# Kernel optimization log

Measured on AMD Instinct MI355X. Metric: run time of the kernel, lower is better.

The kernel has to match this reference:

```python
import jax, jax.numpy as jnp
import numpy as np

EPS = 1e-8  # matches Keras K.l2_normalize epsilon behavior closely enough for fp32

def _l2_normalize(x, axis=-1):
    # Keras l2_normalize: x / sqrt(max(sum(x^2), epsilon))
    sq = jnp.sum(jnp.square(x), axis=axis, keepdims=True)
    return x * jax.lax.rsqrt(jnp.maximum(sq, EPS))

def setup_inputs() -> dict:
    key = jax.random.key(0)
    k1, k2 = jax.random.split(key)
    matrix_1 = jax.random.normal(k1, (8, 2048, 128), dtype=jnp.float32)
    matrix_2 = jax.random.normal(k2, (8, 2048, 128), dtype=jnp.float32)
    return {"matrix_1": matrix_1, "matrix_2": matrix_2}

def reference(matrix_1, matrix_2):
    # Cosine similarity between every row pair: normalize then batched matmul.
    # Mathematically identical to tiling both matrices to (B, R1, R2, D) and
    # computing an elementwise cosine similarity, but without materializing tiles.
    m1 = _l2_normalize(matrix_1, axis=-1)  # (B, R1, D)
    m2 = _l2_normalize(matrix_2, axis=-1)  # (B, R2, D)
    return jnp.einsum('bid,bjd->bij', m1, m2)  # (B, R1, R2)
```

## Files before the change

kernel.cpp:

```cpp
#include <hip/hip_runtime.h>
#include <hip/hip_bf16.h>

#define BATCH 8
#define RROWS 2048
#define DDIM  128
#define BM    128
#define BN    64

using f32x4 = __attribute__((ext_vector_type(4))) float;
using s16x8 = __attribute__((ext_vector_type(8))) short;
using u16x4 = __attribute__((ext_vector_type(4))) unsigned short;

#define SCHED0() __builtin_amdgcn_sched_barrier(0)
#define LGKM0()  asm volatile("s_waitcnt lgkmcnt(0)" ::: "memory")

__device__ __forceinline__ unsigned short f2bf(float f) {
    unsigned int u = __builtin_bit_cast(unsigned int, f);
    u += 0x7fffu + ((u >> 16) & 1u);
    return (unsigned short)(u >> 16);
}

__device__ __forceinline__ u16x4 norm_cvt(float4 v) {
    float s = v.x * v.x + v.y * v.y + v.z * v.z + v.w * v.w;
    #pragma unroll
    for (int i = 1; i <= 16; i <<= 1) s += __shfl_xor(s, i);
    const float r = rsqrtf(fmaxf(s, 1e-8f));
    u16x4 p;
    p[0] = f2bf(v.x * r); p[1] = f2bf(v.y * r);
    p[2] = f2bf(v.z * r); p[3] = f2bf(v.w * r);
    return p;
}

__global__ __launch_bounds__(256, 2) void fused_kernel(const float* __restrict__ m1,
                                                       const float* __restrict__ m2,
                                                       float* __restrict__ out) {
    __shared__ __align__(16) char lds[32768];
    char* Bs0 = lds;
    char* Bs1 = lds + 16384;

    const int tid    = threadIdx.x;
    const int wave   = tid >> 6;
    const int lane   = tid & 63;
    const int l32    = tid & 31;
    const int grp    = tid >> 5;
    const int lid    = blockIdx.x;
    const int b      = lid & 7;
    const int idx    = lid >> 3;
    const int tile_m = idx >> 2;
    const int q      = idx & 3;

    const float* gA = m1 + ((size_t)b * RROWS + (size_t)tile_m * BM) * DDIM;
    const float* gB = m2 + ((size_t)b * RROWS + (size_t)q * 512) * DDIM;

    float4 rb[8];
    #pragma unroll
    for (int i = 0; i < 8; ++i)
        rb[i] = *(const float4*)(gB + (size_t)(i * 8 + grp) * DDIM + l32 * 4);

    #pragma unroll
    for (int s = 0; s < 16; ++s) {
        const int r = s * 8 + grp;
        const float4 va = *(const float4*)(gA + (size_t)r * DDIM + l32 * 4);
        const u16x4 pa = norm_cvt(va);
        const int off = r * 256 + l32 * 8;
        *(u16x4*)(lds + (off ^ ((r & 7) << 4))) = pa;
    }
    LGKM0();
    __builtin_amdgcn_s_barrier();

    const int wr   = wave >> 1;
    const int wc   = wave & 1;
    const int lrow = lane & 15;
    const int kb   = (lane >> 4) * 8;

    s16x8 af[4][4];
    #pragma unroll
    for (int kk = 0; kk < 4; ++kk) {
        const int k = kk * 32 + kb;
        #pragma unroll
        for (int m = 0; m < 4; ++m) {
            const int ra   = wr * 64 + m * 16 + lrow;
            const int offa = ra * 256 + k * 2;
            af[kk][m] = *(const s16x8*)(lds + (offa ^ ((ra & 7) << 4)));
        }
    }
    LGKM0();
    __builtin_amdgcn_s_barrier();

    #pragma unroll
    for (int i = 0; i < 8; ++i) {
        const int r = i * 8 + grp;
        const u16x4 pb = norm_cvt(rb[i]);
        const int off = r * 256 + l32 * 8;
        *(u16x4*)(Bs0 + (off ^ ((r & 7) << 4))) = pb;
    }
    #pragma unroll
    for (int i = 0; i < 8; ++i)
        rb[i] = *(const float4*)(gB + (size_t)(64 + i * 8 + grp) * DDIM + l32 * 4);
    LGKM0();
    __builtin_amdgcn_s_barrier();

    float* gout_base = out + (size_t)b * RROWS * RROWS
                           + (size_t)(tile_m * BM) * RROWS + (size_t)q * 512;

    #pragma unroll
    for (int t = 0; t < 8; ++t) {
        const char* Bs  = (t & 1) ? Bs1 : Bs0;
        char*       Bsn = (t & 1) ? Bs0 : Bs1;

        f32x4 acc[4][2];
        #pragma unroll
        for (int m = 0; m < 4; ++m)
            #pragma unroll
            for (int n = 0; n < 2; ++n)
                acc[m][n] = f32x4{0.f, 0.f, 0.f, 0.f};

        #pragma unroll
        for (int kk = 0; kk < 4; ++kk) {
            const int k = kk * 32 + kb;
            s16x8 bfr[2];
            #pragma unroll
            for (int n = 0; n < 2; ++n) {
                const int rbr  = wc * 32 + n * 16 + lrow;
                const int offb = rbr * 256 + k * 2;
                bfr[n] = *(const s16x8*)(Bs + (offb ^ ((rbr & 7) << 4)));
            }
            #pragma unroll
            for (int m = 0; m < 4; ++m)
                #pragma unroll
                for (int n = 0; n < 2; ++n)
                    acc[m][n] = __builtin_amdgcn_mfma_f32_16x16x32_bf16(af[kk][m], bfr[n], acc[m][n], 0, 0, 0);
        }

        float* gout = gout_base + t * BN;
        const int orow0 = wr * 64 + (lane >> 4) * 4;
        const int ocol0 = wc * 32 + lrow;
        #pragma unroll
        for (int m = 0; m < 4; ++m) {
            #pragma unroll
            for (int n = 0; n < 2; ++n) {
                const int col = ocol0 + n * 16;
                #pragma unroll
                for (int reg = 0; reg < 4; ++reg) {
                    const int row = orow0 + m * 16 + reg;
                    gout[(size_t)row * RROWS + col] = acc[m][n][reg];
                }
            }
        }

        if (t < 7) {
            SCHED0();
            #pragma unroll
            for (int i = 0; i < 8; ++i) {
                const int r = i * 8 + grp;
                const u16x4 pb = norm_cvt(rb[i]);
                const int off = r * 256 + l32 * 8;
                *(u16x4*)(Bsn + (off ^ ((r & 7) << 4))) = pb;
            }
            if (t < 6) {
                #pragma unroll
                for (int i = 0; i < 8; ++i)
                    rb[i] = *(const float4*)(gB + (size_t)((t + 2) * 64 + i * 8 + grp) * DDIM + l32 * 4);
            }
            LGKM0();
            __builtin_amdgcn_s_barrier();
        }
    }
}

extern "C" void kernel_launch(void* const* d_in, const int* in_sizes, int n_in,
                              void* d_out, int out_size, void* d_ws, size_t ws_size,
                              hipStream_t stream) {
    (void)in_sizes; (void)n_in; (void)out_size; (void)d_ws; (void)ws_size;
    const float* m1 = (const float*)d_in[0];
    const float* m2 = (const float*)d_in[1];
    float* out = (float*)d_out;

    fused_kernel<<<dim3(BATCH * (RROWS / BM) * (RROWS / BN / 8)), dim3(256), 0, stream>>>(m1, m2, out);
}
```

Baseline: 32.72 us.

## Double-buffer B register prefetch and normalize next tile before output stores

Splits the B-tile staging registers into two alternating buffers. Each iteration issues the global load for tile t+2 before the MFMA work, then normalizes and writes tile t+1 into LDS before the output stores, with scheduling barriers keeping that order. The goal is more latency hiding for B loads and less time where LDS writes wait behind global stores. In exchange the kernel holds 32 more VGPRs per thread, which could cause spills or hurt occupancy under the launch bounds of 2 blocks.

```diff
diff --git a/kernel.cpp b/kernel.cpp
--- a/kernel.cpp
+++ b/kernel.cpp
@@ -31,6 +31,20 @@
     return p;
 }
 
+#define LOAD_RB(RB, TI)                                                              \
+    _Pragma("unroll")                                                                \
+    for (int i = 0; i < 8; ++i)                                                      \
+        RB[i] = *(const float4*)(gB + (size_t)((TI) * 64 + i * 8 + grp) * DDIM + l32 * 4);
+
+#define PROCESS_RB(RB, DST)                                                          \
+    _Pragma("unroll")                                                                \
+    for (int i = 0; i < 8; ++i) {                                                    \
+        const int r_ = i * 8 + grp;                                                  \
+        const u16x4 pb_ = norm_cvt(RB[i]);                                           \
+        const int off_ = r_ * 256 + l32 * 8;                                         \
+        *(u16x4*)((DST) + (off_ ^ ((r_ & 7) << 4))) = pb_;                           \
+    }
+
 __global__ __launch_bounds__(256, 2) void fused_kernel(const float* __restrict__ m1,
                                                        const float* __restrict__ m2,
                                                        float* __restrict__ out) {
@@ -52,10 +66,8 @@
     const float* gA = m1 + ((size_t)b * RROWS + (size_t)tile_m * BM) * DDIM;
     const float* gB = m2 + ((size_t)b * RROWS + (size_t)q * 512) * DDIM;
 
-    float4 rb[8];
-    #pragma unroll
-    for (int i = 0; i < 8; ++i)
-        rb[i] = *(const float4*)(gB + (size_t)(i * 8 + grp) * DDIM + l32 * 4);
+    float4 rbA[8], rbB[8];
+    LOAD_RB(rbA, 0)
 
     #pragma unroll
     for (int s = 0; s < 16; ++s) {
@@ -87,16 +99,8 @@
     LGKM0();
     __builtin_amdgcn_s_barrier();
 
-    #pragma unroll
-    for (int i = 0; i < 8; ++i) {
-        const int r = i * 8 + grp;
-        const u16x4 pb = norm_cvt(rb[i]);
-        const int off = r * 256 + l32 * 8;
-        *(u16x4*)(Bs0 + (off ^ ((r & 7) << 4))) = pb;
-    }
-    #pragma unroll
-    for (int i = 0; i < 8; ++i)
-        rb[i] = *(const float4*)(gB + (size_t)(64 + i * 8 + grp) * DDIM + l32 * 4);
+    PROCESS_RB(rbA, Bs0)
+    LOAD_RB(rbB, 1)
     LGKM0();
     __builtin_amdgcn_s_barrier();
 
@@ -107,6 +111,12 @@
     for (int t = 0; t < 8; ++t) {
         const char* Bs  = (t & 1) ? Bs1 : Bs0;
         char*       Bsn = (t & 1) ? Bs0 : Bs1;
+
+        if (t < 6) {
+            if ((t & 1) == 0) { LOAD_RB(rbA, t + 2) }
+            else              { LOAD_RB(rbB, t + 2) }
+        }
+        SCHED0();
 
         f32x4 acc[4][2];
         #pragma unroll
@@ -131,6 +141,13 @@
                 for (int n = 0; n < 2; ++n)
                     acc[m][n] = __builtin_amdgcn_mfma_f32_16x16x32_bf16(af[kk][m], bfr[n], acc[m][n], 0, 0, 0);
         }
+        SCHED0();
+
+        if (t < 7) {
+            if (((t + 1) & 1) == 0) { PROCESS_RB(rbA, Bsn) }
+            else                    { PROCESS_RB(rbB, Bsn) }
+        }
+        SCHED0();
 
         float* gout = gout_base + t * BN;
         const int orow0 = wr * 64 + (lane >> 4) * 4;
@@ -149,19 +166,6 @@
         }
 
         if (t < 7) {
-            SCHED0();
-            #pragma unroll
-            for (int i = 0; i < 8; ++i) {
-                const int r = i * 8 + grp;
-                const u16x4 pb = norm_cvt(rb[i]);
-                const int off = r * 256 + l32 * 8;
-                *(u16x4*)(Bsn + (off ^ ((r & 7) << 4))) = pb;
-            }
-            if (t < 6) {
-                #pragma unroll
-                for (int i = 0; i < 8; ++i)
-                    rb[i] = *(const float4*)(gB + (size_t)((t + 2) * 64 + i * 8 + grp) * DDIM + l32 * 4);
-            }
             LGKM0();
             __builtin_amdgcn_s_barrier();
         }
```

After: 34.15 us. 1.04x slower.
